# Optimization experiments

Measured on AMD Instinct MI355X. Metric: run time of the kernel, lower is better.

The kernel has to match this reference:

```python
import jax, jax.numpy as jnp
import numpy as np

T, B, D, R, H = 16, 1024, 1024, 8, 16
DH = D // H


def setup_inputs() -> dict:
    key = jax.random.key(0)
    ks = jax.random.split(key, 10)
    s = 1.0 / np.sqrt(D)
    return {
        "table_embs": jax.random.normal(ks[0], (T, B, D), jnp.float32),
        "rel_embs": jax.random.normal(ks[1], (T, R, D), jnp.float32),
        "rel_idx": jax.random.randint(ks[2], (T, R), 0, T),
        "Wq": jax.random.normal(ks[3], (D, D), jnp.float32) * s,
        "bq": jnp.zeros((D,), jnp.float32),
        "Wk": jax.random.normal(ks[4], (D, D), jnp.float32) * s,
        "bk": jnp.zeros((D,), jnp.float32),
        "Wv": jax.random.normal(ks[5], (D, D), jnp.float32) * s,
        "bv": jnp.zeros((D,), jnp.float32),
        "Wo": jax.random.normal(ks[6], (D, D), jnp.float32) * s,
        "bo": jnp.zeros((D,), jnp.float32),
        "w_rel": jax.random.normal(ks[7], (D,), jnp.float32) * s,
        "b_rel": jnp.zeros((1,), jnp.float32),
    }


def reference(table_embs, rel_embs, rel_idx, Wq, bq, Wk, bk, Wv, bv, Wo, bo, w_rel, b_rel):
    # relationship weights: sigmoid(Linear(rel_emb)) -> scalar per (table, relation)
    rel_w = jax.nn.sigmoid(rel_embs @ w_rel + b_rel[0])          # [T, R]
    # gather related tables' embeddings and apply relationship weight
    others = table_embs[rel_idx]                                  # [T, R, B, D]
    weighted = others * rel_w[:, :, None, None]                   # [T, R, B, D]
    kv_src = jnp.transpose(weighted, (0, 2, 1, 3))                # [T, B, R, D]
    # MultiheadAttention, q_len=1, kv_len=R (PyTorch convention: x @ W.T + b)
    q = (table_embs @ Wq.T + bq).reshape(T, B, H, DH)             # [T, B, H, DH]
    k = (kv_src @ Wk.T + bk).reshape(T, B, R, H, DH)              # [T, B, R, H, DH]
    v = (kv_src @ Wv.T + bv).reshape(T, B, R, H, DH)
    scores = jnp.einsum("tbhd,tbrhd->tbhr", q, k) / np.sqrt(DH)   # [T, B, H, R]
    attn = jax.nn.softmax(scores, axis=-1)
    ctx = jnp.einsum("tbhr,tbrhd->tbhd", attn, v).reshape(T, B, D)
    return ctx @ Wo.T + bo                                        # [T, B, D]
```

## Files before the change

kernel.cpp:

```cpp
#include <hip/hip_runtime.h>


typedef unsigned short u16;
typedef __attribute__((ext_vector_type(8))) short short8;
typedef __attribute__((ext_vector_type(4))) float f32x4;

__device__ __forceinline__ float bf2f(u16 u) {
  unsigned int x = ((unsigned int)u) << 16;
  return __uint_as_float(x);
}
__device__ __forceinline__ u16 f2bf(float f) {
  unsigned int x = __float_as_uint(f);
  unsigned int r = (x + 0x7fffu + ((x >> 16) & 1u)) >> 16;
  return (u16)r;
}

__device__ __forceinline__ void gld_lds16(const void* g, void* l) {
  __builtin_amdgcn_global_load_lds(
      (const __attribute__((address_space(1))) unsigned int*)(unsigned long long)g,
      (__attribute__((address_space(3))) unsigned int*)(unsigned int)(unsigned long long)l,
      16, 0, 0);
}

#define STR_(x) #x
#define STR(x) STR_(x)
#define VWAIT(N) asm volatile("s_waitcnt vmcnt(" STR(N) ")" ::: "memory")
#define LWAIT(N) asm volatile("s_waitcnt lgkmcnt(" STR(N) ")" ::: "memory")
#define SCHED0   __builtin_amdgcn_sched_barrier(0)
#define DSR(dst, base, OFF)                                                    \
  asm volatile("ds_read_b128 %0, %1 offset:" STR(OFF)                          \
               : "=v"(dst) : "v"(base))


__global__ void relw_kernel(const float* __restrict__ rel_embs,
                            const float* __restrict__ w_rel,
                            const float* __restrict__ b_rel,
                            float* __restrict__ rel_w) {
  const int tr = blockIdx.x;
  const float* row = rel_embs + (size_t)tr * 1024;
  const int lane = threadIdx.x;
  float s = 0.f;
  for (int i = lane; i < 1024; i += 64) s += row[i] * w_rel[i];
  for (int off = 32; off > 0; off >>= 1) s += __shfl_down(s, off, 64);
  if (lane == 0) rel_w[tr] = 1.f / (1.f + __expf(-(s + b_rel[0])));
}

__global__ void cvt_f32_bf16(const float* __restrict__ in, u16* __restrict__ out, int n4) {
  int i = blockIdx.x * blockDim.x + threadIdx.x;
  if (i >= n4) return;
  float4 v = ((const float4*)in)[i];
  ushort4 o;
  o.x = f2bf(v.x); o.y = f2bf(v.y); o.z = f2bf(v.z); o.w = f2bf(v.w);
  ((ushort4*)out)[i] = o;
}

__global__ void cvt_w4(const float* __restrict__ Wq, const float* __restrict__ Wk,
                       const float* __restrict__ Wv, const float* __restrict__ Wo,
                       u16* __restrict__ Wcat, u16* __restrict__ Wob) {
  const int i = blockIdx.x * 256 + threadIdx.x;
  const int w = i >> 18;
  const int j = i & 0x3ffff;
  const float* src = (w == 0) ? Wq : (w == 1) ? Wk : (w == 2) ? Wv : Wo;
  u16* dst = (w == 3) ? Wob : (Wcat + ((size_t)w << 20));
  float4 v = ((const float4*)src)[j];
  ushort4 o;
  o.x = f2bf(v.x); o.y = f2bf(v.y); o.z = f2bf(v.z); o.w = f2bf(v.w);
  ((ushort4*)dst)[j] = o;
}


__device__ __forceinline__ void mainloop256(const u16* __restrict__ A,
                                            const u16* __restrict__ B,
                                            u16* lds, int m0, int n0,
                                            f32x4 (&acc)[8][4]) {
  const int tid  = threadIdx.x;
  const int lane = tid & 63;
  const int w    = tid >> 6;
  const int wm   = w >> 2, wn = w & 3;
  const int fr   = lane & 15, fq = lane >> 4;
  const int swz  = fr & 7;

  const unsigned A0 = 0, B0 = 16384, A1 = 32768, B1 = 49152;

  const int srow = tid >> 3;
  const int lc   = (tid & 7) ^ (srow & 7);
  const u16* a0p = A + (size_t)(m0 + srow) * 1024 + lc * 8;
  const u16* b0p = B + (size_t)(n0 + srow) * 1024 + lc * 8;
  const unsigned d0 = (unsigned)((tid & ~63) * 8);

  unsigned uA0k0, uA0k1, uA1k0, uA1k1, uB0k0, uB0k1, uB1k0, uB1k1;
  {
    const unsigned ck0 = (unsigned)(((0 + fq) ^ swz) << 3);
    const unsigned ck1 = (unsigned)(((4 + fq) ^ swz) << 3);
    const unsigned ar = (unsigned)((wm * 128 + fr) * 64);
    const unsigned br = (unsigned)((wn * 64 + fr) * 64);
    uA0k0 = (A0 + ar + ck0) * 2;  uA0k1 = (A0 + ar + ck1) * 2;
    uA1k0 = (A1 + ar + ck0) * 2;  uA1k1 = (A1 + ar + ck1) * 2;
    uB0k0 = (B0 + br + ck0) * 2;  uB0k1 = (B0 + br + ck1) * 2;
    uB1k0 = (B1 + br + ck0) * 2;  uB1k1 = (B1 + br + ck1) * 2;
  }

  short8 afA[4], afB[4], bfr[2][8];

#define STAGE_B4(BO)                                                           \
  do {                                                                         \
    gld_lds16(b0p + 0 * 65536, lds + (BO) + d0 + 0 * 4096);                    \
    gld_lds16(b0p + 1 * 65536, lds + (BO) + d0 + 1 * 4096);                    \
    gld_lds16(b0p + 2 * 65536, lds + (BO) + d0 + 2 * 4096);                    \
    gld_lds16(b0p + 3 * 65536, lds + (BO) + d0 + 3 * 4096);                    \
    b0p += 64;                                                                 \
  } while (0)

#define STAGE_A2(ra, rb, AO)                                                   \
  do {                                                                         \
    gld_lds16(a0p + (ra) * 65536, lds + (AO) + d0 + (ra) * 4096);              \
    gld_lds16(a0p + (rb) * 65536, lds + (AO) + d0 + (rb) * 4096);              \
  } while (0)

#define RD_A2(dst, bk0, bk1, O0, O1)                                           \
  do {                                                                         \
    DSR(dst[0], bk0, O0); DSR(dst[1], bk0, O1);                                \
    DSR(dst[2], bk1, O0); DSR(dst[3], bk1, O1);                                \
  } while (0)

#define RD_B2(TB, bk0, bk1, O0, O1, I0)                                        \
  do {                                                                         \
    DSR(bfr[TB][(I0)+0], bk0, O0); DSR(bfr[TB][(I0)+1], bk1, O0);              \
    DSR(bfr[TB][(I0)+2], bk0, O1); DSR(bfr[TB][(I0)+3], bk1, O1);              \
  } while (0)

#define MFMA_PH(q, S, TB)                                                      \
  do {                                                                         \
    __builtin_amdgcn_s_setprio(1);                                             \
    _Pragma("unroll")                                                          \
    for (int j = 0; j < 4; ++j) {                                              \
      acc[2*(q)][j]   = __builtin_amdgcn_mfma_f32_16x16x32_bf16(S[0], bfr[TB][2*j], acc[2*(q)][j],   0, 0, 0); \
      acc[2*(q)+1][j] = __builtin_amdgcn_mfma_f32_16x16x32_bf16(S[1], bfr[TB][2*j], acc[2*(q)+1][j], 0, 0, 0); \
    }                                                                          \
    _Pragma("unroll")                                                          \
    for (int j = 0; j < 4; ++j) {                                              \
      acc[2*(q)][j]   = __builtin_amdgcn_mfma_f32_16x16x32_bf16(S[2], bfr[TB][2*j+1], acc[2*(q)][j],   0, 0, 0); \
      acc[2*(q)+1][j] = __builtin_amdgcn_mfma_f32_16x16x32_bf16(S[3], bfr[TB][2*j+1], acc[2*(q)+1][j], 0, 0, 0); \
    }                                                                          \
    __builtin_amdgcn_s_setprio(0);                                             \
  } while (0)

#define BAR __builtin_amdgcn_s_barrier()

#define KTILE(aC0, aC1, aN0, aN1, bN0, bN1, TBC, TBN, AO_N, BO_N)              \
  do {                                                                         \
                         \
    RD_A2(afB, aC0, aC1, 4096, 6144);                                          \
    STAGE_B4(BO_N);                                                            \
    LWAIT(4); SCHED0;                                                          \
    MFMA_PH(0, afA, TBC); SCHED0;                                              \
    VWAIT(4);                                         \
    BAR;                                                                       \
                        \
    RD_A2(afA, aC0, aC1, 8192, 10240);                                         \
    STAGE_A2(0, 2, AO_N);                                                      \
    LWAIT(4); SCHED0;                                                          \
    MFMA_PH(1, afB, TBC); SCHED0;                                              \
    VWAIT(2);                                               \
    BAR;                                                                       \
         \
    RD_A2(afB, aC0, aC1, 12288, 14336);                                        \
    RD_B2(TBN, bN0, bN1, 0, 2048, 0);                                          \
    STAGE_A2(1, 3, AO_N); a0p += 64;                                           \
    LWAIT(8); SCHED0;                                                          \
    MFMA_PH(2, afA, TBC); SCHED0;                                              \
    VWAIT(2);                                         \
    BAR;                                                                       \
                   \
    RD_A2(afA, aN0, aN1, 0, 2048);                                             \
    RD_B2(TBN, bN0, bN1, 4096, 6144, 4);                                       \
    LWAIT(8); SCHED0;                                                          \
    MFMA_PH(3, afB, TBC); SCHED0;                                              \
    BAR;                                                                       \
  } while (0)

#define KTILE_LAST(aC0, aC1, TBC)                                              \
  do {                                                                         \
    RD_A2(afB, aC0, aC1, 4096, 6144);                                          \
    LWAIT(4); SCHED0;                                                          \
    MFMA_PH(0, afA, TBC); SCHED0;                                              \
    VWAIT(0);                                                                  \
    BAR;                                                                       \
    RD_A2(afA, aC0, aC1, 8192, 10240);                                         \
    LWAIT(4); SCHED0;                                                          \
    MFMA_PH(1, afB, TBC); SCHED0;                                              \
    BAR;                                                                       \
    RD_A2(afB, aC0, aC1, 12288, 14336);                                        \
    LWAIT(4); SCHED0;                                                          \
    MFMA_PH(2, afA, TBC); SCHED0;                                              \
    BAR;                                                                       \
    LWAIT(0); SCHED0;                                                          \
    MFMA_PH(3, afB, TBC);                                                      \
  } while (0)

  gld_lds16(b0p + 0 * 65536, lds + B0 + d0 + 0 * 4096);
  gld_lds16(b0p + 1 * 65536, lds + B0 + d0 + 1 * 4096);
  gld_lds16(b0p + 2 * 65536, lds + B0 + d0 + 2 * 4096);
  gld_lds16(b0p + 3 * 65536, lds + B0 + d0 + 3 * 4096);
  gld_lds16(a0p + 0 * 65536, lds + A0 + d0 + 0 * 4096);
  gld_lds16(a0p + 2 * 65536, lds + A0 + d0 + 2 * 4096);
  gld_lds16(a0p + 1 * 65536, lds + A0 + d0 + 1 * 4096);
  gld_lds16(a0p + 3 * 65536, lds + A0 + d0 + 3 * 4096);
  a0p += 64; b0p += 64;
  VWAIT(2);
  BAR;
  RD_B2(0, uB0k0, uB0k1, 0, 2048, 0);
  RD_B2(0, uB0k0, uB0k1, 4096, 6144, 4);
  RD_A2(afA, uA0k0, uA0k1, 0, 2048);

  for (int it = 0; it < 7; ++it) {
    KTILE(uA0k0, uA0k1, uA1k0, uA1k1, uB1k0, uB1k1, 0, 1, A1, B1);
    KTILE(uA1k0, uA1k1, uA0k0, uA0k1, uB0k0, uB0k1, 1, 0, A0, B0);
  }
  KTILE(uA0k0, uA0k1, uA1k0, uA1k1, uB1k0, uB1k1, 0, 1, A1, B1);
  KTILE_LAST(uA1k0, uA1k1, 1);

#undef STAGE_B4
#undef STAGE_A2
#undef RD_A2
#undef RD_B2
#undef MFMA_PH
#undef BAR
#undef KTILE
#undef KTILE_LAST
}

__device__ __forceinline__ void xcd_swizzle(int nx, int ny, int& bx, int& by) {
  const int nwg = nx * ny;
  int bid = by * nx + bx;
  bid = (bid & 7) * (nwg >> 3) + (bid >> 3);
  bx = bid % nx;
  by = bid / nx;
}

__global__ __launch_bounds__(512, 1)
void gemm_qkv(const u16* __restrict__ A, const u16* __restrict__ Bw,
              const float* __restrict__ bq,
              u16* __restrict__ Qt, u16* __restrict__ Kt, u16* __restrict__ Vt) {
  __shared__ __align__(16) u16 lds[65536];
  int bx = blockIdx.x, by = blockIdx.y;
  xcd_swizzle(gridDim.x, gridDim.y, bx, by);
  const int n0 = bx * 256;
  const int m0 = by * 256;
  f32x4 acc[8][4];
#pragma unroll
  for (int i = 0; i < 8; ++i)
#pragma unroll
    for (int j = 0; j < 4; ++j) acc[i][j] = (f32x4){0.f, 0.f, 0.f, 0.f};

  mainloop256(A, Bw, lds, m0, n0, acc);
  __syncthreads();

  const int tid  = threadIdx.x;
  const int lane = tid & 63;
  const int w    = tid >> 6;
  const int wm   = w >> 2, wn = w & 3;
  const int colw = lane & 15, roww = (lane >> 4) * 4;
  const int t = m0 >> 10, b0 = m0 & 1023;
  const int sel = n0 >> 10, dbase = n0 & 1023;
  u16* outp = (sel == 0) ? Qt : (sel == 1) ? Kt : Vt;

  {
    char* reg = (char*)(lds + wm * 32768);
#pragma unroll
    for (int j = 0; j < 4; ++j) {
      const int dl = wn * 64 + j * 16 + colw;
      const float badd = (sel == 0) ? bq[dbase + dl] : 0.f;
      char* rowp = reg + (unsigned)dl * 256;
      const unsigned sx = ((unsigned)dl & 7) << 4;
#pragma unroll
      for (int i = 0; i < 8; ++i) {
        const int bl = i * 16 + roww;
        uint2 pv;
        pv.x = (unsigned)f2bf(acc[i][j][0] + badd)
             | ((unsigned)f2bf(acc[i][j][1] + badd) << 16);
        pv.y = (unsigned)f2bf(acc[i][j][2] + badd)
             | ((unsigned)f2bf(acc[i][j][3] + badd) << 16);
        *(uint2*)(rowp + (((unsigned)bl * 2) ^ sx)) = pv;
      }
    }
  }
  __syncthreads();
#pragma unroll
  for (int pass = 0; pass < 2; ++pass) {
    const char* regp = (const char*)(lds + pass * 32768);
#pragma unroll
    for (int rr = 0; rr < 8; ++rr) {
      const int slot = rr * 512 + tid;
      const int row = slot >> 4, c16 = slot & 15;
      const uint4 v = *(const uint4*)(regp + (unsigned)row * 256
                                      + (((unsigned)c16 * 16) ^ (((unsigned)row & 7) << 4)));
      *(uint4*)(outp + ((size_t)t << 20) + (size_t)(dbase + row) * 1024
                + b0 + pass * 128 + c16 * 8) = v;
    }
  }
}

__global__ __launch_bounds__(512, 1)
void gemm_out(const u16* __restrict__ A, const u16* __restrict__ Bw,
              const float* __restrict__ bo, float* __restrict__ out) {
  __shared__ __align__(16) u16 lds[65536];
  int bx = blockIdx.x, by = blockIdx.y;
  xcd_swizzle(gridDim.x, gridDim.y, bx, by);
  const int n0 = bx * 256;
  const int m0 = by * 256;
  f32x4 acc[8][4];
#pragma unroll
  for (int i = 0; i < 8; ++i)
#pragma unroll
    for (int j = 0; j < 4; ++j) acc[i][j] = (f32x4){0.f, 0.f, 0.f, 0.f};

  mainloop256(A, Bw, lds, m0, n0, acc);

  const int lane = threadIdx.x & 63;
  const int w    = threadIdx.x >> 6;
  const int wm   = w >> 2, wn = w & 3;
  const int colw = lane & 15, roww = (lane >> 4) * 4;
#pragma unroll
  for (int j = 0; j < 4; ++j) {
    const int gn = n0 + wn * 64 + j * 16 + colw;
    const float bov = bo[gn];
#pragma unroll
    for (int i = 0; i < 8; ++i) {
      const int gm = m0 + wm * 128 + i * 16 + roww;
#pragma unroll
      for (int r = 0; r < 4; ++r)
        out[(size_t)(gm + r) * 1024 + gn] = acc[i][j][r] + bov;
    }
  }
}

__global__ __launch_bounds__(256)
void attn5(const u16* __restrict__ Qt, const u16* __restrict__ Kt,
           const u16* __restrict__ Vt,
           const float* __restrict__ relw, const int* __restrict__ rel_idx,
           const float* __restrict__ bk, const float* __restrict__ bv,
           u16* __restrict__ ctx) {
  const int tid = threadIdx.x;
  const int h = blockIdx.y, t = blockIdx.z;
  const int b0 = blockIdx.x * 256;
  const int b = b0 + tid;
  const int hd = h * 64;

  __shared__ u16  st[256 * 34];
  __shared__ float bks[64], bvs[64], rws[8];
  __shared__ int   rids[8];

  if (tid < 64) { bks[tid] = bk[hd + tid]; bvs[tid] = bv[hd + tid]; }
  else if (tid < 72) { rws[tid - 64] = relw[t * 8 + (tid - 64)];
                       rids[tid - 64] = rel_idx[t * 8 + (tid - 64)]; }
  __syncthreads();

  const unsigned qoff = ((unsigned)t << 20) + ((unsigned)hd << 10) + (unsigned)b;
  unsigned koff[8];
#pragma unroll
  for (int r = 0; r < 8; ++r)
    koff[r] = ((unsigned)rids[r] << 20) + ((unsigned)hd << 10) + (unsigned)b;

  float acc[8];
#pragma unroll
  for (int r = 0; r < 8; ++r) acc[r] = 0.f;
  float qbk = 0.f;
#pragma unroll 4
  for (int d = 0; d < 64; ++d) {
    const float q = bf2f(Qt[qoff + d * 1024]);
    qbk += q * bks[d];
#pragma unroll
    for (int r = 0; r < 8; ++r)
      acc[r] += q * bf2f(Kt[koff[r] + d * 1024]);
  }

  float w[8];
  {
    float s[8], mx = -1e30f;
#pragma unroll
    for (int r = 0; r < 8; ++r) {
      s[r] = (rws[r] * acc[r] + qbk) * 0.125f;
      mx = fmaxf(mx, s[r]);
    }
    float sum = 0.f;
#pragma unroll
    for (int r = 0; r < 8; ++r) { s[r] = __expf(s[r] - mx); sum += s[r]; }
    const float inv = 1.f / sum;
#pragma unroll
    for (int r = 0; r < 8; ++r) w[r] = s[r] * inv * rws[r];
  }

  for (int half = 0; half < 2; ++half) {
#pragma unroll
    for (int dp = 0; dp < 32; dp += 2) {
      const int d = half * 32 + dp;
      float o0 = bvs[d];
      float o1 = bvs[d + 1];
#pragma unroll
      for (int r = 0; r < 8; ++r) {
        o0 += w[r] * bf2f(Vt[koff[r] + d * 1024]);
        o1 += w[r] * bf2f(Vt[koff[r] + (d + 1) * 1024]);
      }
      const unsigned p = (unsigned)f2bf(o0) | ((unsigned)f2bf(o1) << 16);
      *(unsigned*)(st + tid * 34 + dp) = p;
    }
    __syncthreads();
    {
      const int sub = tid & 7;
      const int rbase = tid >> 3;
#pragma unroll
      for (int p = 0; p < 8; ++p) {
        const int row = p * 32 + rbase;
        const uint2 v = *(const uint2*)(st + row * 34 + sub * 4);
        *(uint2*)(ctx + ((size_t)(t * 1024 + b0 + row)) * 1024
                  + hd + half * 32 + sub * 4) = v;
      }
    }
    __syncthreads();
  }
}


extern "C" void kernel_launch(void* const* d_in, const int* in_sizes, int n_in,
                              void* d_out, int out_size, void* d_ws, size_t ws_size,
                              hipStream_t stream) {
  const float* table = (const float*)d_in[0];
  const float* rele  = (const float*)d_in[1];
  const int*   ridx  = (const int*)d_in[2];
  const float* Wq    = (const float*)d_in[3];
  const float* bq    = (const float*)d_in[4];
  const float* Wk    = (const float*)d_in[5];
  const float* bk    = (const float*)d_in[6];
  const float* Wv    = (const float*)d_in[7];
  const float* bv    = (const float*)d_in[8];
  const float* Wo    = (const float*)d_in[9];
  const float* bo    = (const float*)d_in[10];
  const float* wr    = (const float*)d_in[11];
  const float* br    = (const float*)d_in[12];
  float* out = (float*)d_out;

  char* ws = (char*)d_ws;
  const size_t MB = 1024 * 1024;
  u16*  Xbf  = (u16*)(ws);
  u16*  Kt   = (u16*)(ws + 32  * MB);
  u16*  Vt   = (u16*)(ws + 64  * MB);
  u16*  Qt   = (u16*)(ws + 96  * MB);
  u16*  Wcat = (u16*)(ws + 128 * MB);
  u16*  Wob  = (u16*)(ws + 134 * MB);
  float* relw = (float*)(ws + 136 * MB);
  u16*  ctxb = Xbf;

  relw_kernel<<<128, 64, 0, stream>>>(rele, wr, br, relw);
  cvt_f32_bf16<<<16384, 256, 0, stream>>>(table, Xbf, 4194304);
  cvt_w4<<<4096, 256, 0, stream>>>(Wq, Wk, Wv, Wo, Wcat, Wob);

  gemm_qkv<<<dim3(12, 64), 512, 0, stream>>>(Xbf, Wcat, bq, Qt, Kt, Vt);
  attn5<<<dim3(4, 16, 16), 256, 0, stream>>>(Qt, Kt, Vt, relw, ridx, bk, bv, ctxb);
  gemm_out<<<dim3(4, 64), 512, 0, stream>>>(ctxb, Wob, bo, out);
}
```

Measured before the change: 371.7 us.

## Rework attention kernel: two batch rows per thread, direct vector stores, remapped grid

The attention kernel now gives each thread two adjacent batch rows, so Q, K and V are read with 32-bit loads instead of 16-bit ones. Output goes straight to global memory as 16-byte vector stores per row, dropping the LDS transpose staging and its barriers. The grid is flattened to 256 blocks of 512 threads, with a custom head/table mapping that may aid L2 locality. The costs are fewer blocks, more registers per thread, and strided (non-coalesced across lanes) context stores, since each thread writes its own row.

```diff
diff --git a/kernel.cpp b/kernel.cpp
--- a/kernel.cpp
+++ b/kernel.cpp
@@ -9,6 +9,8 @@
   unsigned int x = ((unsigned int)u) << 16;
   return __uint_as_float(x);
 }
+__device__ __forceinline__ float lo_f(unsigned v) { return __uint_as_float(v << 16); }
+__device__ __forceinline__ float hi_f(unsigned v) { return __uint_as_float(v & 0xffff0000u); }
 __device__ __forceinline__ u16 f2bf(float f) {
   unsigned int x = __float_as_uint(f);
   unsigned int r = (x + 0x7fffu + ((x >> 16) & 1u)) >> 16;
@@ -335,89 +337,104 @@
   }
 }
 
-__global__ __launch_bounds__(256)
-void attn5(const u16* __restrict__ Qt, const u16* __restrict__ Kt,
+__global__ __launch_bounds__(512)
+void attn6(const u16* __restrict__ Qt, const u16* __restrict__ Kt,
            const u16* __restrict__ Vt,
            const float* __restrict__ relw, const int* __restrict__ rel_idx,
            const float* __restrict__ bk, const float* __restrict__ bv,
            u16* __restrict__ ctx) {
   const int tid = threadIdx.x;
-  const int h = blockIdx.y, t = blockIdx.z;
-  const int b0 = blockIdx.x * 256;
-  const int b = b0 + tid;
+  const int bid = blockIdx.x;
+  const int h = (bid & 7) * 2 + ((bid >> 3) >> 4);
+  const int t = (bid >> 3) & 15;
   const int hd = h * 64;
-
-  __shared__ u16  st[256 * 34];
+  const int b0 = tid * 2;
+
   __shared__ float bks[64], bvs[64], rws[8];
   __shared__ int   rids[8];
-
   if (tid < 64) { bks[tid] = bk[hd + tid]; bvs[tid] = bv[hd + tid]; }
   else if (tid < 72) { rws[tid - 64] = relw[t * 8 + (tid - 64)];
                        rids[tid - 64] = rel_idx[t * 8 + (tid - 64)]; }
   __syncthreads();
 
-  const unsigned qoff = ((unsigned)t << 20) + ((unsigned)hd << 10) + (unsigned)b;
+  const unsigned qoff = ((unsigned)t << 20) + ((unsigned)hd << 10) + (unsigned)b0;
   unsigned koff[8];
 #pragma unroll
   for (int r = 0; r < 8; ++r)
-    koff[r] = ((unsigned)rids[r] << 20) + ((unsigned)hd << 10) + (unsigned)b;
-
-  float acc[8];
-#pragma unroll
-  for (int r = 0; r < 8; ++r) acc[r] = 0.f;
-  float qbk = 0.f;
+    koff[r] = ((unsigned)rids[r] << 20) + ((unsigned)hd << 10) + (unsigned)b0;
+
+  float a0[8], a1[8];
+#pragma unroll
+  for (int r = 0; r < 8; ++r) { a0[r] = 0.f; a1[r] = 0.f; }
+  float qbk0 = 0.f, qbk1 = 0.f;
 #pragma unroll 4
   for (int d = 0; d < 64; ++d) {
-    const float q = bf2f(Qt[qoff + d * 1024]);
-    qbk += q * bks[d];
-#pragma unroll
-    for (int r = 0; r < 8; ++r)
-      acc[r] += q * bf2f(Kt[koff[r] + d * 1024]);
-  }
-
-  float w[8];
+    const unsigned qv = *(const unsigned*)(Qt + qoff + d * 1024);
+    const float q0 = lo_f(qv), q1 = hi_f(qv);
+    qbk0 += q0 * bks[d];
+    qbk1 += q1 * bks[d];
+#pragma unroll
+    for (int r = 0; r < 8; ++r) {
+      const unsigned kv = *(const unsigned*)(Kt + koff[r] + d * 1024);
+      a0[r] += q0 * lo_f(kv);
+      a1[r] += q1 * hi_f(kv);
+    }
+  }
+
+  float w0[8], w1[8];
   {
-    float s[8], mx = -1e30f;
+    float s0[8], s1[8], m0 = -1e30f, m1 = -1e30f;
 #pragma unroll
     for (int r = 0; r < 8; ++r) {
-      s[r] = (rws[r] * acc[r] + qbk) * 0.125f;
-      mx = fmaxf(mx, s[r]);
-    }
-    float sum = 0.f;
-#pragma unroll
-    for (int r = 0; r < 8; ++r) { s[r] = __expf(s[r] - mx); sum += s[r]; }
-    const float inv = 1.f / sum;
-#pragma unroll
-    for (int r = 0; r < 8; ++r) w[r] = s[r] * inv * rws[r];
-  }
-
-  for (int half = 0; half < 2; ++half) {
-#pragma unroll
-    for (int dp = 0; dp < 32; dp += 2) {
-      const int d = half * 32 + dp;
-      float o0 = bvs[d];
-      float o1 = bvs[d + 1];
+      s0[r] = (rws[r] * a0[r] + qbk0) * 0.125f;
+      s1[r] = (rws[r] * a1[r] + qbk1) * 0.125f;
+      m0 = fmaxf(m0, s0[r]);
+      m1 = fmaxf(m1, s1[r]);
+    }
+    float t0 = 0.f, t1 = 0.f;
+#pragma unroll
+    for (int r = 0; r < 8; ++r) {
+      s0[r] = __expf(s0[r] - m0); t0 += s0[r];
+      s1[r] = __expf(s1[r] - m1); t1 += s1[r];
+    }
+    const float i0 = 1.f / t0, i1 = 1.f / t1;
+#pragma unroll
+    for (int r = 0; r < 8; ++r) {
+      w0[r] = s0[r] * i0 * rws[r];
+      w1[r] = s1[r] * i1 * rws[r];
+    }
+  }
+
+  u16* cp0 = ctx + ((size_t)(t * 1024 + b0)) * 1024 + hd;
+  u16* cp1 = cp0 + 1024;
+  for (int dblk = 0; dblk < 8; ++dblk) {
+    float o0[8], o1[8];
+#pragma unroll
+    for (int dp = 0; dp < 8; ++dp) {
+      const float bvv = bvs[dblk * 8 + dp];
+      o0[dp] = bvv; o1[dp] = bvv;
+    }
+#pragma unroll
+    for (int dp = 0; dp < 8; ++dp) {
+      const int d = dblk * 8 + dp;
 #pragma unroll
       for (int r = 0; r < 8; ++r) {
-        o0 += w[r] * bf2f(Vt[koff[r] + d * 1024]);
-        o1 += w[r] * bf2f(Vt[koff[r] + (d + 1) * 1024]);
+        const unsigned vv = *(const unsigned*)(Vt + koff[r] + d * 1024);
+        o0[dp] += w0[r] * lo_f(vv);
+        o1[dp] += w1[r] * hi_f(vv);
       }
-      const unsigned p = (unsigned)f2bf(o0) | ((unsigned)f2bf(o1) << 16);
-      *(unsigned*)(st + tid * 34 + dp) = p;
-    }
-    __syncthreads();
-    {
-      const int sub = tid & 7;
-      const int rbase = tid >> 3;
-#pragma unroll
-      for (int p = 0; p < 8; ++p) {
-        const int row = p * 32 + rbase;
-        const uint2 v = *(const uint2*)(st + row * 34 + sub * 4);
-        *(uint2*)(ctx + ((size_t)(t * 1024 + b0 + row)) * 1024
-                  + hd + half * 32 + sub * 4) = v;
-      }
-    }
-    __syncthreads();
+    }
+    uint4 pv0, pv1;
+    pv0.x = (unsigned)f2bf(o0[0]) | ((unsigned)f2bf(o0[1]) << 16);
+    pv0.y = (unsigned)f2bf(o0[2]) | ((unsigned)f2bf(o0[3]) << 16);
+    pv0.z = (unsigned)f2bf(o0[4]) | ((unsigned)f2bf(o0[5]) << 16);
+    pv0.w = (unsigned)f2bf(o0[6]) | ((unsigned)f2bf(o0[7]) << 16);
+    pv1.x = (unsigned)f2bf(o1[0]) | ((unsigned)f2bf(o1[1]) << 16);
+    pv1.y = (unsigned)f2bf(o1[2]) | ((unsigned)f2bf(o1[3]) << 16);
+    pv1.z = (unsigned)f2bf(o1[4]) | ((unsigned)f2bf(o1[5]) << 16);
+    pv1.w = (unsigned)f2bf(o1[6]) | ((unsigned)f2bf(o1[7]) << 16);
+    *(uint4*)(cp0 + dblk * 8) = pv0;
+    *(uint4*)(cp1 + dblk * 8) = pv1;
   }
 }
 
@@ -456,6 +473,6 @@
   cvt_w4<<<4096, 256, 0, stream>>>(Wq, Wk, Wv, Wo, Wcat, Wob);
 
   gemm_qkv<<<dim3(12, 64), 512, 0, stream>>>(Xbf, Wcat, bq, Qt, Kt, Vt);
-  attn5<<<dim3(4, 16, 16), 256, 0, stream>>>(Qt, Kt, Vt, relw, ridx, bk, bv, ctxb);
+  attn6<<<256, 512, 0, stream>>>(Qt, Kt, Vt, relw, ridx, bk, bv, ctxb);
   gemm_out<<<dim3(4, 64), 512, 0, stream>>>(ctxb, Wob, bo, out);
 }
```

Result: faster. 363.8 us (-2.1%).
